# Kernel optimization log

Measured on AMD Instinct MI355X. Metric: run time of the kernel, lower is better.

The kernel has to match this reference:

```python
import jax, jax.numpy as jnp
import numpy as np

EMBED = 1024
HEADS = 16
HEAD_DIM = EMBED // HEADS


def setup_inputs() -> dict:
    key = jax.random.key(0)
    ks = jax.random.split(key, 12)
    B, S, E = 2, 2048, EMBED
    scale = 1.0 / np.sqrt(E)
    inp = {
        "query": jax.random.normal(ks[0], (B, S, E), jnp.float32),
        "key": jax.random.normal(ks[1], (B, S, E), jnp.float32),
        "value": jax.random.normal(ks[2], (B, S, E), jnp.float32),
        "Wq": jax.random.normal(ks[3], (E, E), jnp.float32) * scale,
        "bq": jax.random.normal(ks[4], (E,), jnp.float32) * 0.01,
        "Wk": jax.random.normal(ks[5], (E, E), jnp.float32) * scale,
        "bk": jax.random.normal(ks[6], (E,), jnp.float32) * 0.01,
        "Wv": jax.random.normal(ks[7], (E, E), jnp.float32) * scale,
        "bv": jax.random.normal(ks[8], (E,), jnp.float32) * 0.01,
        "Wo": jax.random.normal(ks[9], (E, E), jnp.float32) * scale,
        "bo": jax.random.normal(ks[10], (E,), jnp.float32) * 0.01,
    }
    return inp


def reference(query, key, value, Wq, bq, Wk, bk, Wv, bv, Wo, bo):
    B, Sq, E = query.shape
    Sk = key.shape[1]
    H, D = HEADS, HEAD_DIM
    # QKV projections (torch Linear: x @ W.T + b)
    q = (query @ Wq.T + bq).reshape(B, Sq, H, D)
    k = (key @ Wk.T + bk).reshape(B, Sk, H, D)
    v = (value @ Wv.T + bv).reshape(B, Sk, H, D)
    # energy: [B, H, Sq, Sk]; note scale = 1/sqrt(embed_size), not head_dim
    energy = jnp.einsum("bqhd,bkhd->bhqk", q, k)
    scale = jnp.asarray(E, energy.dtype) ** 0.5
    attn = jax.nn.softmax(energy / scale, axis=-1)
    out = jnp.einsum("bhqk,bkhd->bqhd", attn, v).reshape(B, Sq, E)
    # fc_out (dropout is identity at eval)
    return out @ Wo.T + bo
```

## Files before the change

### kernel.cpp

```cpp
#include <hip/hip_runtime.h>
#include <hip/hip_bf16.h>

typedef __hip_bfloat16 bf16;
typedef short frag8 __attribute__((ext_vector_type(8)));
typedef _Float16 half4 __attribute__((ext_vector_type(4)));
typedef float f32x4 __attribute__((ext_vector_type(4)));

typedef __attribute__((address_space(3))) void lds_void;
typedef __attribute__((address_space(1))) const void gbl_void;

__device__ __forceinline__ void gld16(const void* g, void* l) {
  __builtin_amdgcn_global_load_lds((gbl_void*)g, (lds_void*)l, 16, 0, 0);
}

__device__ __forceinline__ unsigned short f2bf(float f) {
  union { float f; unsigned u; } x; x.f = f;
  unsigned r = x.u + 0x7FFFu + ((x.u >> 16) & 1u);
  return (unsigned short)(r >> 16);
}

#define QSCALE 0.0450842200278f
#define MFIX 4.0f

struct CvtArgs {
  const float4* src[4];
  ushort4* dst[4];
};
__global__ __launch_bounds__(256) void cvt_all(CvtArgs a) {
  const int t = blockIdx.y;
  const int i = blockIdx.x * 256 + threadIdx.x;
  float4 v = a.src[t][i];
  ushort4 o;
  o.x = f2bf(v.x); o.y = f2bf(v.y); o.z = f2bf(v.z); o.w = f2bf(v.w);
  a.dst[t][i] = o;
}

template<int MODE>
__global__ __launch_bounds__(256)
void gemm_bt(const void* __restrict__ A0, const void* __restrict__ A1, const void* __restrict__ A2,
             const bf16* __restrict__ W0, const bf16* __restrict__ W1, const bf16* __restrict__ W2,
             const float* __restrict__ b0, const float* __restrict__ b1, const float* __restrict__ b2,
             void* __restrict__ o0, void* __restrict__ o1, void* __restrict__ o2) {
  constexpr int NK = 1024;
  constexpr int BM = (MODE == 1) ? 128 : 64;
  __shared__ __align__(16) bf16 As[2][BM * 32];
  __shared__ __align__(16) bf16 Bs[2][128 * 32];
  const int tid = threadIdx.x;
  const int wave = tid >> 6, lane = tid & 63, quad = lane >> 4, l16 = lane & 15;
  const int wm = wave >> 1, wn = wave & 1;
  const int bm = blockIdx.x, bn = blockIdx.y;

  const void* A = A0; const bf16* W = W0; const float* bias = b0; void* out = o0;
  int z = 0;
  if constexpr (MODE == 1) {
    z = blockIdx.z;
    if (z == 1) { A = A1; W = W1; bias = b1; out = o1; }
    else if (z == 2) { A = A2; W = W2; bias = b2; out = o2; }
  }

  const bf16* Wb = W + (size_t)bn * 128 * NK;
  const int c0_ = tid & 3, r0_ = tid >> 2;

  auto stageW = [&](int k0, int buf) {
    #pragma unroll
    for (int is = 0; is < 2; ++is) {
      const int c = tid + is * 256;
      const int r = r0_ + is * 64;
      const int gc = (c0_ ^ (r & 3)) << 3;
      gld16(Wb + (size_t)r * NK + k0 + gc, (void*)(&Bs[buf][(size_t)c * 8]));
    }
  };

  const int rc = (quad ^ (l16 & 3)) << 3;

  if constexpr (MODE == 0) {
    const bf16* Ab16 = (const bf16*)A + (size_t)bm * 64 * NK;
    f32x4 acc[8];
    #pragma unroll
    for (int j = 0; j < 8; ++j) acc[j] = (f32x4){0.f, 0.f, 0.f, 0.f};

    auto stageA = [&](int k0, int buf) {
      const int r = r0_;
      const int gc = (c0_ ^ (r & 3)) << 3;
      gld16(Ab16 + (size_t)r * NK + k0 + gc, (void*)(&As[buf][(size_t)tid * 8]));
    };

    stageA(0, 0); stageW(0, 0);
    #pragma unroll 2
    for (int kt = 0; kt < 32; ++kt) {
      __syncthreads();
      if (kt < 31) { stageA((kt + 1) * 32, (kt + 1) & 1); stageW((kt + 1) * 32, (kt + 1) & 1); }
      const bf16* as_ = As[kt & 1];
      const bf16* bs_ = Bs[kt & 1];
      frag8 af = *(const frag8*)&as_[(wave * 16 + l16) * 32 + rc];
      #pragma unroll
      for (int j = 0; j < 8; ++j) {
        frag8 bf_ = *(const frag8*)&bs_[(j * 16 + l16) * 32 + rc];
        acc[j] = __builtin_amdgcn_mfma_f32_16x16x32_bf16(af, bf_, acc[j], 0, 0, 0);
      }
    }
    #pragma unroll
    for (int j = 0; j < 8; ++j) {
      const int col = bn * 128 + j * 16 + l16;
      const float bv = bias[col];
      #pragma unroll
      for (int r = 0; r < 4; ++r) {
        const int row = bm * 64 + wave * 16 + quad * 4 + r;
        ((float*)out)[(size_t)row * 1024 + col] = acc[j][r] + bv;
      }
    }
  } else {
    const float* Abf = (const float*)A + (size_t)bm * 128 * NK;
    f32x4 acc[4][4];
    #pragma unroll
    for (int i = 0; i < 4; ++i)
      #pragma unroll
      for (int j = 0; j < 4; ++j)
        acc[i][j] = (f32x4){0.f, 0.f, 0.f, 0.f};

    float4 alo[2][2], ahi[2][2];
    auto loadA = [&](int k0, int set) {
      #pragma unroll
      for (int is = 0; is < 2; ++is) {
        const int r = r0_ + is * 64;
        const int gc = (c0_ ^ (r & 3)) << 3;
        const float* p = Abf + (size_t)r * NK + k0 + gc;
        alo[set][is] = *(const float4*)p;
        ahi[set][is] = *(const float4*)(p + 4);
      }
    };
    auto writeA = [&](int set, int buf) {
      #pragma unroll
      for (int is = 0; is < 2; ++is) {
        const int c = tid + is * 256;
        ushort4 w0, w1;
        w0.x = f2bf(alo[set][is].x); w0.y = f2bf(alo[set][is].y);
        w0.z = f2bf(alo[set][is].z); w0.w = f2bf(alo[set][is].w);
        w1.x = f2bf(ahi[set][is].x); w1.y = f2bf(ahi[set][is].y);
        w1.z = f2bf(ahi[set][is].z); w1.w = f2bf(ahi[set][is].w);
        ushort* d = (ushort*)&As[buf][(size_t)c * 8];
        *(ushort4*)d = w0;
        *(ushort4*)(d + 4) = w1;
      }
    };

    loadA(0, 0); stageW(0, 0);
    writeA(0, 0);
    loadA(32, 1);
    #pragma unroll 2
    for (int kt = 0; kt < 32; ++kt) {
      __syncthreads();
      if (kt < 31) {
        stageW((kt + 1) * 32, (kt + 1) & 1);
        writeA((kt + 1) & 1, (kt + 1) & 1);
      }
      if (kt < 30) loadA((kt + 2) * 32, kt & 1);
      const bf16* as_ = As[kt & 1];
      const bf16* bs_ = Bs[kt & 1];
      frag8 af[4], bfr[4];
      #pragma unroll
      for (int i = 0; i < 4; ++i)
        af[i] = *(const frag8*)&as_[(wm * 64 + i * 16 + l16) * 32 + rc];
      #pragma unroll
      for (int j = 0; j < 4; ++j)
        bfr[j] = *(const frag8*)&bs_[(wn * 64 + j * 16 + l16) * 32 + rc];
      #pragma unroll
      for (int i = 0; i < 4; ++i)
        #pragma unroll
        for (int j = 0; j < 4; ++j)
          acc[i][j] = __builtin_amdgcn_mfma_f32_16x16x32_bf16(af[i], bfr[j], acc[i][j], 0, 0, 0);
    }

    #pragma unroll
    for (int j = 0; j < 4; ++j) {
      const int col = bn * 128 + wn * 64 + j * 16 + l16;
      const float bv = bias[col];
      #pragma unroll
      for (int i = 0; i < 4; ++i) {
        #pragma unroll
        for (int r = 0; r < 4; ++r) {
          const int row = bm * 128 + wm * 64 + i * 16 + quad * 4 + r;
          float v = acc[i][j][r] + bv;
          const int b = row >> 11, s = row & 2047;
          const int hh = col >> 6, d = col & 63;
          const size_t bh = (size_t)(b * 16 + hh);
          if (z == 0) {
            v *= QSCALE;
            ((bf16*)out)[(bh * 2048 + s) * 64 + d] = __float2bfloat16(v);
          } else if (z == 1) {
            const int rr = s & 127;
            const size_t addr = bh * 131072 + (size_t)(s >> 7) * 8192 + (size_t)rr * 64
                              + (size_t)(((d >> 3) ^ (rr & 7)) << 3) + (d & 7);
            ((bf16*)out)[addr] = __float2bfloat16(v);
          } else {
            const int kvl = s & 127;
            const size_t addr = bh * 131072 + (size_t)(s >> 7) * 8192 + (size_t)d * 128
                              + (size_t)((((kvl >> 2) ^ (d & 15)) << 2)) + (kvl & 3);
            ((_Float16*)out)[addr] = (_Float16)v;
          }
        }
      }
    }
  }
}

__global__ __launch_bounds__(256)
void flash_attn(const bf16* __restrict__ Q, const bf16* __restrict__ K,
                const _Float16* __restrict__ Vt, bf16* __restrict__ ctx) {
  __shared__ __align__(16) bf16 Ks[2][128 * 64];
  __shared__ __align__(16) _Float16 Vs[2][64 * 128];
  const int tid = threadIdx.x;
  const int wave = tid >> 6, lane = tid & 63, quad = lane >> 4, l16 = lane & 15;
  const int bh = blockIdx.x, b = bh >> 4, h = bh & 15;
  const int q0 = blockIdx.y * 128 + wave * 32;
  const bf16* Qb = Q + (size_t)bh * 2048 * 64;
  const bf16* Kb = K + (size_t)bh * 131072;
  const _Float16* Vb = Vt + (size_t)bh * 131072;

  frag8 qf[2][2];
  #pragma unroll
  for (int qt = 0; qt < 2; ++qt)
    #pragma unroll
    for (int ks = 0; ks < 2; ++ks)
      qf[qt][ks] = *(const frag8*)(Qb + (size_t)(q0 + qt * 16 + l16) * 64 + ks * 32 + quad * 8);

  f32x4 rsv[2];
  f32x4 o[2][4];
  #pragma unroll
  for (int qt = 0; qt < 2; ++qt) {
    rsv[qt] = (f32x4){0.f, 0.f, 0.f, 0.f};
    #pragma unroll
    for (int dt = 0; dt < 4; ++dt)
      o[qt][dt] = (f32x4){0.f, 0.f, 0.f, 0.f};
  }

  const int xk = l16 & 7;

  auto stage = [&](int kt, int buf) {
    #pragma unroll
    for (int is = 0; is < 4; ++is) {
      const int c = tid + is * 256;
      gld16(Kb + (size_t)kt * 8192 + (size_t)c * 8, (void*)(&Ks[buf][(size_t)c * 8]));
      gld16(Vb + (size_t)kt * 8192 + (size_t)c * 8, (void*)(&Vs[buf][(size_t)c * 8]));
    }
  };

  stage(0, 0);
  #pragma unroll 2
  for (int kt = 0; kt < 16; ++kt) {
    __syncthreads();
    if (kt < 15) stage(kt + 1, (kt + 1) & 1);
    const bf16* ks_ = Ks[kt & 1];
    const _Float16* vs_ = Vs[kt & 1];

    f32x4 s[2][8];
    #pragma unroll
    for (int qt = 0; qt < 2; ++qt)
      #pragma unroll
      for (int jt = 0; jt < 8; ++jt)
        s[qt][jt] = (f32x4){-MFIX, -MFIX, -MFIX, -MFIX};
    #pragma unroll
    for (int ks = 0; ks < 2; ++ks) {
      frag8 kf[8];
      #pragma unroll
      for (int jt = 0; jt < 8; ++jt)
        kf[jt] = *(const frag8*)&ks_[(jt * 16 + l16) * 64 + (((ks * 4 + quad) ^ xk) << 3)];
      #pragma unroll
      for (int qt = 0; qt < 2; ++qt)
        #pragma unroll
        for (int jt = 0; jt < 8; ++jt)
          s[qt][jt] = __builtin_amdgcn_mfma_f32_16x16x32_bf16(kf[jt], qf[qt][ks], s[qt][jt], 0, 0, 0);
    }

    half4 pf[2][8];
    #pragma unroll
    for (int qt = 0; qt < 2; ++qt) {
      #pragma unroll
      for (int jt = 0; jt < 8; ++jt) {
        f32x4 p4;
        #pragma unroll
        for (int r = 0; r < 4; ++r)
          p4[r] = __builtin_amdgcn_exp2f(s[qt][jt][r]);
        rsv[qt] += p4;
        #pragma unroll
        for (int r = 0; r < 4; ++r)
          pf[qt][jt][r] = (_Float16)p4[r];
      }
    }

    #pragma unroll
    for (int jt = 0; jt < 8; ++jt) {
      half4 vf[4];
      #pragma unroll
      for (int dt = 0; dt < 4; ++dt)
        vf[dt] = *(const half4*)&vs_[(dt * 16 + l16) * 128 + (((jt * 4 + quad) ^ l16) << 2)];
      #pragma unroll
      for (int qt = 0; qt < 2; ++qt)
        #pragma unroll
        for (int dt = 0; dt < 4; ++dt)
          o[qt][dt] = __builtin_amdgcn_mfma_f32_16x16x16f16(vf[dt], pf[qt][jt], o[qt][dt], 0, 0, 0);
    }
  }

  #pragma unroll
  for (int qt = 0; qt < 2; ++qt) {
    float l = rsv[qt][0] + rsv[qt][1] + rsv[qt][2] + rsv[qt][3];
    l += __shfl_xor(l, 16, 64);
    l += __shfl_xor(l, 32, 64);
    const float inv = __builtin_amdgcn_rcpf(l);
    const int q = q0 + qt * 16 + l16;
    #pragma unroll
    for (int dt = 0; dt < 4; ++dt) {
      ushort4 w;
      w.x = f2bf(o[qt][dt][0] * inv);
      w.y = f2bf(o[qt][dt][1] * inv);
      w.z = f2bf(o[qt][dt][2] * inv);
      w.w = f2bf(o[qt][dt][3] * inv);
      const int d = dt * 16 + quad * 4;
      *(uint2*)&ctx[((size_t)(b * 2048 + q)) * 1024 + h * 64 + d] = *(uint2*)&w;
    }
  }
}

extern "C" void kernel_launch(void* const* d_in, const int* in_sizes, int n_in,
                              void* d_out, int out_size, void* d_ws, size_t ws_size,
                              hipStream_t stream) {
  const float* q_in = (const float*)d_in[0];
  const float* k_in = (const float*)d_in[1];
  const float* v_in = (const float*)d_in[2];
  const float* Wq = (const float*)d_in[3];
  const float* bq = (const float*)d_in[4];
  const float* Wk = (const float*)d_in[5];
  const float* bk = (const float*)d_in[6];
  const float* Wv = (const float*)d_in[7];
  const float* bv = (const float*)d_in[8];
  const float* Wo = (const float*)d_in[9];
  const float* bo = (const float*)d_in[10];

  char* ws = (char*)d_ws;
  const size_t MB = 1024 * 1024;
  bf16* Wqb = (bf16*)(ws + 0 * MB);
  bf16* Wkb = (bf16*)(ws + 2 * MB);
  bf16* Wvb = (bf16*)(ws + 4 * MB);
  bf16* Wob = (bf16*)(ws + 6 * MB);
  bf16* Qw  = (bf16*)(ws + 8 * MB);
  bf16* Kw  = (bf16*)(ws + 16 * MB);
  _Float16* Vtw = (_Float16*)(ws + 24 * MB);
  bf16* Ctx = (bf16*)(ws + 32 * MB);

  {
    CvtArgs a;
    a.src[0] = (const float4*)Wq; a.dst[0] = (ushort4*)Wqb;
    a.src[1] = (const float4*)Wk; a.dst[1] = (ushort4*)Wkb;
    a.src[2] = (const float4*)Wv; a.dst[2] = (ushort4*)Wvb;
    a.src[3] = (const float4*)Wo; a.dst[3] = (ushort4*)Wob;
    cvt_all<<<dim3(1024, 4), 256, 0, stream>>>(a);
  }

  gemm_bt<1><<<dim3(32, 8, 3), 256, 0, stream>>>(q_in, k_in, v_in, Wqb, Wkb, Wvb,
                                                 bq, bk, bv, Qw, Kw, (void*)Vtw);
  flash_attn<<<dim3(32, 16), 256, 0, stream>>>(Qw, Kw, Vtw, Ctx);
  gemm_bt<0><<<dim3(64, 8, 1), 256, 0, stream>>>(Ctx, nullptr, nullptr, Wob, nullptr, nullptr,
                                                 bo, nullptr, nullptr, d_out, nullptr, nullptr);
}
```

Before: 253.5 us.

## Replace LDS-direct loads with register-staged triple-buffered prefetch in GEMMs

Both GEMM modes now load W (and the bf16 A tile) into registers with plain global loads instead of global_load_lds. They keep a three-deep register ring that prefetches two k-steps ahead, then write to double-buffered LDS after each barrier. The fp32 A conversion now packs eight bf16 values into one 16-byte LDS store, the k-loop is fully unrolled, and launch bounds request two blocks per CU. This is meant to hide global memory latency better, at the cost of more registers and extra VGPR-to-LDS write instructions.

Result: slower. 329.3 us (+29.9%).

```diff
diff --git a/kernel.cpp b/kernel.cpp
--- a/kernel.cpp
+++ b/kernel.cpp
@@ -13,10 +13,20 @@
   __builtin_amdgcn_global_load_lds((gbl_void*)g, (lds_void*)l, 16, 0, 0);
 }
 
-__device__ __forceinline__ unsigned short f2bf(float f) {
+__device__ __forceinline__ unsigned f2bf(float f) {
   union { float f; unsigned u; } x; x.f = f;
   unsigned r = x.u + 0x7FFFu + ((x.u >> 16) & 1u);
-  return (unsigned short)(r >> 16);
+  return r >> 16;
+}
+__device__ __forceinline__ unsigned short f2bf16(float f) { return (unsigned short)f2bf(f); }
+
+__device__ __forceinline__ uint4 pack8(float4 lo, float4 hi) {
+  uint4 o;
+  o.x = f2bf(lo.x) | (f2bf(lo.y) << 16);
+  o.y = f2bf(lo.z) | (f2bf(lo.w) << 16);
+  o.z = f2bf(hi.x) | (f2bf(hi.y) << 16);
+  o.w = f2bf(hi.z) | (f2bf(hi.w) << 16);
+  return o;
 }
 
 #define QSCALE 0.0450842200278f
@@ -31,12 +41,12 @@
   const int i = blockIdx.x * 256 + threadIdx.x;
   float4 v = a.src[t][i];
   ushort4 o;
-  o.x = f2bf(v.x); o.y = f2bf(v.y); o.z = f2bf(v.z); o.w = f2bf(v.w);
+  o.x = f2bf16(v.x); o.y = f2bf16(v.y); o.z = f2bf16(v.z); o.w = f2bf16(v.w);
   a.dst[t][i] = o;
 }
 
 template<int MODE>
-__global__ __launch_bounds__(256)
+__global__ __launch_bounds__(256, 2)
 void gemm_bt(const void* __restrict__ A0, const void* __restrict__ A1, const void* __restrict__ A2,
              const bf16* __restrict__ W0, const bf16* __restrict__ W1, const bf16* __restrict__ W2,
              const float* __restrict__ b0, const float* __restrict__ b1, const float* __restrict__ b2,
@@ -60,36 +70,47 @@
 
   const bf16* Wb = W + (size_t)bn * 128 * NK;
   const int c0_ = tid & 3, r0_ = tid >> 2;
-
-  auto stageW = [&](int k0, int buf) {
+  const int rc = (quad ^ (l16 & 3)) << 3;
+
+  uint4 wreg[3][2];
+  auto loadW = [&](int k0, int set) {
     #pragma unroll
     for (int is = 0; is < 2; ++is) {
-      const int c = tid + is * 256;
       const int r = r0_ + is * 64;
       const int gc = (c0_ ^ (r & 3)) << 3;
-      gld16(Wb + (size_t)r * NK + k0 + gc, (void*)(&Bs[buf][(size_t)c * 8]));
+      wreg[set][is] = *(const uint4*)(Wb + (size_t)r * NK + k0 + gc);
     }
   };
-
-  const int rc = (quad ^ (l16 & 3)) << 3;
+  auto writeW = [&](int set, int buf) {
+    #pragma unroll
+    for (int is = 0; is < 2; ++is)
+      *(uint4*)&Bs[buf][(size_t)(tid + is * 256) * 8] = wreg[set][is];
+  };
 
   if constexpr (MODE == 0) {
     const bf16* Ab16 = (const bf16*)A + (size_t)bm * 64 * NK;
+    uint4 areg[3];
+    auto loadA = [&](int k0, int set) {
+      const int gc = (c0_ ^ (r0_ & 3)) << 3;
+      areg[set] = *(const uint4*)(Ab16 + (size_t)r0_ * NK + k0 + gc);
+    };
+    auto writeA = [&](int set, int buf) {
+      *(uint4*)&As[buf][(size_t)tid * 8] = areg[set];
+    };
+
     f32x4 acc[8];
     #pragma unroll
     for (int j = 0; j < 8; ++j) acc[j] = (f32x4){0.f, 0.f, 0.f, 0.f};
 
-    auto stageA = [&](int k0, int buf) {
-      const int r = r0_;
-      const int gc = (c0_ ^ (r & 3)) << 3;
-      gld16(Ab16 + (size_t)r * NK + k0 + gc, (void*)(&As[buf][(size_t)tid * 8]));
-    };
-
-    stageA(0, 0); stageW(0, 0);
-    #pragma unroll 2
+    loadA(0, 0); loadW(0, 0);
+    loadA(32, 1); loadW(32, 1);
+    writeA(0, 0); writeW(0, 0);
+    loadA(64, 2); loadW(64, 2);
+    #pragma unroll
     for (int kt = 0; kt < 32; ++kt) {
       __syncthreads();
-      if (kt < 31) { stageA((kt + 1) * 32, (kt + 1) & 1); stageW((kt + 1) * 32, (kt + 1) & 1); }
+      if (kt < 31) { writeA((kt + 1) % 3, (kt + 1) & 1); writeW((kt + 1) % 3, (kt + 1) & 1); }
+      if (kt < 29) { loadA((kt + 3) * 32, kt % 3); loadW((kt + 3) * 32, kt % 3); }
       const bf16* as_ = As[kt & 1];
       const bf16* bs_ = Bs[kt & 1];
       frag8 af = *(const frag8*)&as_[(wave * 16 + l16) * 32 + rc];
@@ -111,14 +132,7 @@
     }
   } else {
     const float* Abf = (const float*)A + (size_t)bm * 128 * NK;
-    f32x4 acc[4][4];
-    #pragma unroll
-    for (int i = 0; i < 4; ++i)
-      #pragma unroll
-      for (int j = 0; j < 4; ++j)
-        acc[i][j] = (f32x4){0.f, 0.f, 0.f, 0.f};
-
-    float4 alo[2][2], ahi[2][2];
+    float4 alo[3][2], ahi[3][2];
     auto loadA = [&](int k0, int set) {
       #pragma unroll
       for (int is = 0; is < 2; ++is) {
@@ -131,30 +145,26 @@
     };
     auto writeA = [&](int set, int buf) {
       #pragma unroll
-      for (int is = 0; is < 2; ++is) {
-        const int c = tid + is * 256;
-        ushort4 w0, w1;
-        w0.x = f2bf(alo[set][is].x); w0.y = f2bf(alo[set][is].y);
-        w0.z = f2bf(alo[set][is].z); w0.w = f2bf(alo[set][is].w);
-        w1.x = f2bf(ahi[set][is].x); w1.y = f2bf(ahi[set][is].y);
-        w1.z = f2bf(ahi[set][is].z); w1.w = f2bf(ahi[set][is].w);
-        ushort* d = (ushort*)&As[buf][(size_t)c * 8];
-        *(ushort4*)d = w0;
-        *(ushort4*)(d + 4) = w1;
-      }
+      for (int is = 0; is < 2; ++is)
+        *(uint4*)&As[buf][(size_t)(tid + is * 256) * 8] = pack8(alo[set][is], ahi[set][is]);
     };
 
-    loadA(0, 0); stageW(0, 0);
-    writeA(0, 0);
-    loadA(32, 1);
-    #pragma unroll 2
+    f32x4 acc[4][4];
+    #pragma unroll
+    for (int i = 0; i < 4; ++i)
+      #pragma unroll
+      for (int j = 0; j < 4; ++j)
+        acc[i][j] = (f32x4){0.f, 0.f, 0.f, 0.f};
+
+    loadA(0, 0); loadW(0, 0);
+    loadA(32, 1); loadW(32, 1);
+    writeA(0, 0); writeW(0, 0);
+    loadA(64, 2); loadW(64, 2);
+    #pragma unroll
     for (int kt = 0; kt < 32; ++kt) {
       __syncthreads();
-      if (kt < 31) {
-        stageW((kt + 1) * 32, (kt + 1) & 1);
-        writeA((kt + 1) & 1, (kt + 1) & 1);
-      }
-      if (kt < 30) loadA((kt + 2) * 32, kt & 1);
+      if (kt < 31) { writeA((kt + 1) % 3, (kt + 1) & 1); writeW((kt + 1) % 3, (kt + 1) & 1); }
+      if (kt < 29) { loadA((kt + 3) * 32, kt % 3); loadW((kt + 3) * 32, kt % 3); }
       const bf16* as_ = As[kt & 1];
       const bf16* bs_ = Bs[kt & 1];
       frag8 af[4], bfr[4];
@@ -312,10 +322,10 @@
     #pragma unroll
     for (int dt = 0; dt < 4; ++dt) {
       ushort4 w;
-      w.x = f2bf(o[qt][dt][0] * inv);
-      w.y = f2bf(o[qt][dt][1] * inv);
-      w.z = f2bf(o[qt][dt][2] * inv);
-      w.w = f2bf(o[qt][dt][3] * inv);
+      w.x = f2bf16(o[qt][dt][0] * inv);
+      w.y = f2bf16(o[qt][dt][1] * inv);
+      w.z = f2bf16(o[qt][dt][2] * inv);
+      w.w = f2bf16(o[qt][dt][3] * inv);
       const int d = dt * 16 + quad * 4;
       *(uint2*)&ctx[((size_t)(b * 2048 + q)) * 1024 + h * 64 + d] = *(uint2*)&w;
     }
```
